# Kernel optimization log

Measured on AMD Instinct MI355X. Metric: run time of the kernel, lower is better.

Reference implementation:

```python
import jax, jax.numpy as jnp
import numpy as np

B, L, D_MODEL = 4, 4096, 1024
D_STATE = 16
DT_RANK = D_MODEL // 16  # 64
K = 4  # conv kernel size
EPS = 1e-5


def setup_inputs() -> dict:
    key = jax.random.key(0)
    ks = jax.random.split(key, 8)
    s = 0.02
    f = jax.random.normal(ks[0], (B, L, D_MODEL), dtype=jnp.float32)
    ln_g = jnp.ones((D_MODEL,), jnp.float32)
    ln_b = jnp.zeros((D_MODEL,), jnp.float32)
    Wx = jax.random.normal(ks[1], (D_MODEL, D_MODEL), jnp.float32) * s
    bx = jnp.zeros((D_MODEL,), jnp.float32)
    conv_w = jax.random.normal(ks[2], (D_MODEL, K), jnp.float32) * 0.1
    conv_b = jax.random.normal(ks[3], (D_MODEL,), jnp.float32) * s
    Wxp = jax.random.normal(ks[4], (D_MODEL, DT_RANK + 2 * D_STATE), jnp.float32) * s
    Wdt = jax.random.normal(ks[5], (DT_RANK, D_MODEL), jnp.float32) * s
    # negative bias keeps delta small so the (non-exponentiated) recurrence
    # h = (delta*A)*h + ... stays stable over L=4096 steps (|delta*A| < 1)
    bdt = jnp.full((D_MODEL,), -4.0, jnp.float32)
    A_log = jnp.tile(jnp.log(jnp.arange(1, D_STATE + 1, dtype=jnp.float32)), (D_MODEL, 1))
    Dp = jnp.ones((D_MODEL,), jnp.float32)
    return {"f": f, "ln_g": ln_g, "ln_b": ln_b, "Wx": Wx, "bx": bx,
            "conv_w": conv_w, "conv_b": conv_b, "Wxp": Wxp, "Wdt": Wdt,
            "bdt": bdt, "A_log": A_log, "Dp": Dp}


def reference(f, ln_g, ln_b, Wx, bx, conv_w, conv_b, Wxp, Wdt, bdt, A_log, Dp):
    b, l, d = f.shape
    # LayerNorm
    mu = jnp.mean(f, axis=-1, keepdims=True)
    var = jnp.mean(jnp.square(f - mu), axis=-1, keepdims=True)
    fn = (f - mu) * jax.lax.rsqrt(var + EPS) * ln_g + ln_b
    # input projection
    x = fn @ Wx + bx  # (b, l, d)
    # depthwise causal conv1d (torch pad=3 both sides then truncate to l == left-pad 3)
    xp = jnp.pad(x, ((0, 0), (K - 1, 0), (0, 0)))
    windows = jnp.stack([xp[:, k:k + l, :] for k in range(K)], axis=-1)  # (b, l, d, k)
    x = jnp.einsum('bldk,dk->bld', windows, conv_w) + conv_b
    x = jax.nn.silu(x)
    # selective SSM
    x_dbl = x @ Wxp  # (b, l, dt_rank + 2*n)
    dt = x_dbl[..., :DT_RANK]
    Bm = x_dbl[..., DT_RANK:DT_RANK + D_STATE]
    Cm = x_dbl[..., DT_RANK + D_STATE:]
    delta = jax.nn.softplus(dt @ Wdt + bdt)  # (b, l, d)
    A = -jnp.exp(A_log)  # (d, n)

    def step(h, inp):
        d_t, B_t, C_t, x_t = inp  # (b,d) (b,n) (b,n) (b,d)
        dA = d_t[:, :, None] * A                                  # (b, d, n)
        dB = (d_t * x_t)[:, :, None] * B_t[:, None, :]            # (b, d, n)
        h = dA * h + dB
        y = jnp.einsum('bdn,bn->bd', h, C_t)
        return h, y

    h0 = jnp.zeros((b, d, D_STATE), x.dtype)
    xs = (jnp.swapaxes(delta, 0, 1), jnp.swapaxes(Bm, 0, 1),
          jnp.swapaxes(Cm, 0, 1), jnp.swapaxes(x, 0, 1))
    _, ys = jax.lax.scan(step, h0, xs)  # ys: (l, b, d)
    y = jnp.swapaxes(ys, 0, 1) + x * Dp
    return y
```

## Files before the change

kernel.cpp:

```cpp
#include <hip/hip_runtime.h>
#include <cstdint>
#include <cstddef>

#define D_MODEL 1024
#define SEQ_L   4096
#define BATCH   4
#define NROWS   (BATCH*SEQ_L)
#define DSTATE  16
#define DTRANK  64
#define NDBL    96
#define CLEN    64
#define WARM    16
#define CT      16

typedef __attribute__((ext_vector_type(8))) _Float16 f16x8;
typedef __attribute__((ext_vector_type(4))) _Float16 h4;
typedef __attribute__((ext_vector_type(8))) _Float16 h8;
typedef __attribute__((ext_vector_type(4))) float f32x4;
typedef __attribute__((ext_vector_type(2))) float f32x2;

__device__ __forceinline__ float silu(float v) {
  return v / (1.f + __expf(-v));
}

__device__ __forceinline__ float softplus(float z) {
  return (z > 20.f) ? z : __logf(1.f + __expf(z));
}

__device__ __forceinline__ int swz64(int r, int e) { return e ^ ((r & 7) << 3); }

__global__ __launch_bounds__(256) void ln_kernel(const float* __restrict__ f,
                                                 const float* __restrict__ g,
                                                 const float* __restrict__ bta,
                                                 _Float16* __restrict__ fnb) {
  int row = blockIdx.x;
  int tid = threadIdx.x;
  const float* fr = f + (size_t)row * D_MODEL;
  float4 v = *(const float4*)&fr[tid * 4];
  float s  = v.x + v.y + v.z + v.w;
  float ss = v.x*v.x + v.y*v.y + v.z*v.z + v.w*v.w;
  #pragma unroll
  for (int o = 32; o > 0; o >>= 1) { s += __shfl_down(s, o); ss += __shfl_down(ss, o); }
  __shared__ float rs[8];
  int lane = tid & 63, w = tid >> 6;
  if (lane == 0) { rs[w] = s; rs[4 + w] = ss; }
  __syncthreads();
  if (tid == 0) {
    float S = rs[0] + rs[1] + rs[2] + rs[3];
    float SS = rs[4] + rs[5] + rs[6] + rs[7];
    float mu = S * (1.f / D_MODEL);
    float var = SS * (1.f / D_MODEL) - mu * mu;
    rs[0] = mu; rs[1] = rsqrtf(var + 1e-5f);
  }
  __syncthreads();
  float mu = rs[0], rstd = rs[1];
  float4 gv = *(const float4*)&g[tid * 4];
  float4 bv = *(const float4*)&bta[tid * 4];
  h4 o;
  o.x = (_Float16)((v.x - mu) * rstd * gv.x + bv.x);
  o.y = (_Float16)((v.y - mu) * rstd * gv.y + bv.y);
  o.z = (_Float16)((v.z - mu) * rstd * gv.z + bv.z);
  o.w = (_Float16)((v.w - mu) * rstd * gv.w + bv.w);
  *(h4*)&fnb[(size_t)row * D_MODEL + tid * 4] = o;
}

__global__ __launch_bounds__(256) void tcast(const float* __restrict__ W,
                                             _Float16* __restrict__ Wt,
                                             int rows, int cols) {
  __shared__ float tile[32][33];
  int tx = threadIdx.x & 31, ty = threadIdx.x >> 5;
  int c0 = blockIdx.x * 32, r0 = blockIdx.y * 32;
  #pragma unroll
  for (int i = 0; i < 4; ++i) {
    int r = ty + i * 8;
    tile[r][tx] = W[(size_t)(r0 + r) * cols + c0 + tx];
  }
  __syncthreads();
  #pragma unroll
  for (int i = 0; i < 4; ++i) {
    int n = ty + i * 8;
    Wt[(size_t)(c0 + n) * rows + r0 + tx] = (_Float16)tile[tx][n];
  }
}

__global__ __launch_bounds__(256, 4) void gemm1(const _Float16* __restrict__ Ab,
                                                const _Float16* __restrict__ Bt,
                                                const float* __restrict__ bias,
                                                _Float16* __restrict__ C) {
  __shared__ __align__(16) _Float16 As[128 * 64];
  __shared__ __align__(16) _Float16 Bs[128 * 64];
  const int K = D_MODEL, N = D_MODEL;
  int tid = threadIdx.x;
  int row0 = blockIdx.x * 128;
  int col0 = blockIdx.y * 128;
  int wave = tid >> 6, lane = tid & 63;
  int wr = wave >> 1, wc = wave & 1;
  int lr = lane & 15, half = lane >> 4;
  f32x4 acc[4][4] = {};

  int r_[4], gofs[4], wofs[4];
  #pragma unroll
  for (int i = 0; i < 4; ++i) {
    int c = tid + i * 256;
    int r = c >> 3, kc = c & 7;
    r_[i] = r;
    gofs[i] = kc * 8;
    wofs[i] = r * 64 + ((kc ^ (r & 7)) * 8);
  }

  for (int ks = 0; ks < 16; ++ks) {
    int k0 = ks * 64;
    h8 av[4], bv[4];
    #pragma unroll
    for (int i = 0; i < 4; ++i) {
      av[i] = *(const h8*)&Ab[(size_t)(row0 + r_[i]) * K + k0 + gofs[i]];
      bv[i] = *(const h8*)&Bt[(size_t)(col0 + r_[i]) * K + k0 + gofs[i]];
    }
    __syncthreads();
    #pragma unroll
    for (int i = 0; i < 4; ++i) {
      *(h8*)&As[wofs[i]] = av[i];
      *(h8*)&Bs[wofs[i]] = bv[i];
    }
    __syncthreads();
    #pragma unroll
    for (int kk = 0; kk < 2; ++kk) {
      int kch = ((kk * 4 + half) ^ (lr & 7)) * 8;
      f16x8 a[4], b[4];
      #pragma unroll
      for (int m = 0; m < 4; ++m)
        a[m] = *(const f16x8*)&As[(wr * 64 + m * 16 + lr) * 64 + kch];
      #pragma unroll
      for (int n = 0; n < 4; ++n)
        b[n] = *(const f16x8*)&Bs[(wc * 64 + n * 16 + lr) * 64 + kch];
      #pragma unroll
      for (int m = 0; m < 4; ++m)
        #pragma unroll
        for (int n = 0; n < 4; ++n)
          acc[m][n] = __builtin_amdgcn_mfma_f32_16x16x32_f16(b[n], a[m], acc[m][n], 0, 0, 0);
    }
  }
  #pragma unroll
  for (int m = 0; m < 4; ++m) {
    int gr = row0 + wr * 64 + m * 16 + lr;
    #pragma unroll
    for (int n = 0; n < 4; ++n) {
      int gc = col0 + wc * 64 + n * 16 + half * 4;
      float4 bv4 = *(const float4*)&bias[gc];
      h4 o;
      o.x = (_Float16)(acc[m][n][0] + bv4.x);
      o.y = (_Float16)(acc[m][n][1] + bv4.y);
      o.z = (_Float16)(acc[m][n][2] + bv4.z);
      o.w = (_Float16)(acc[m][n][3] + bv4.w);
      *(h4*)&C[(size_t)gr * N + gc] = o;
    }
  }
}

__global__ __launch_bounds__(256) void conv_silu(const _Float16* __restrict__ xlin,
                                                 const float* __restrict__ cw,
                                                 const float* __restrict__ cb,
                                                 _Float16* __restrict__ xo) {
  int idx = blockIdx.x * 256 + threadIdx.x;
  int d8 = idx & 127;
  int tg = idx >> 7;
  int row0 = tg * CT;
  int l0 = row0 & (SEQ_L - 1);
  int d = d8 * 8;
  float w[8][4];
  #pragma unroll
  for (int j = 0; j < 8; ++j) {
    float4 t = *(const float4*)&cw[(d + j) * 4];
    w[j][0] = t.x; w[j][1] = t.y; w[j][2] = t.z; w[j][3] = t.w;
  }
  float bias[8];
  #pragma unroll
  for (int j = 0; j < 8; j += 4) {
    float4 cbv = *(const float4*)&cb[d + j];
    bias[j] = cbv.x; bias[j+1] = cbv.y; bias[j+2] = cbv.z; bias[j+3] = cbv.w;
  }
  float win0[8], win1[8], win2[8];
  if (l0 == 0) {
    #pragma unroll
    for (int j = 0; j < 8; ++j) { win0[j] = 0.f; win1[j] = 0.f; win2[j] = 0.f; }
  } else {
    h8 m3 = *(const h8*)&xlin[(size_t)(row0 - 3) * D_MODEL + d];
    h8 m2 = *(const h8*)&xlin[(size_t)(row0 - 2) * D_MODEL + d];
    h8 m1 = *(const h8*)&xlin[(size_t)(row0 - 1) * D_MODEL + d];
    #pragma unroll
    for (int j = 0; j < 8; ++j) { win0[j] = (float)m3[j]; win1[j] = (float)m2[j]; win2[j] = (float)m1[j]; }
  }
  #pragma unroll
  for (int tt = 0; tt < CT; tt += 4) {
    h8 ld[4];
    #pragma unroll
    for (int k = 0; k < 4; ++k)
      ld[k] = *(const h8*)&xlin[(size_t)(row0 + tt + k) * D_MODEL + d];
    #pragma unroll
    for (int k = 0; k < 4; ++k) {
      float cur[8];
      #pragma unroll
      for (int j = 0; j < 8; ++j) cur[j] = (float)ld[k][j];
      h8 o;
      #pragma unroll
      for (int j = 0; j < 8; ++j) {
        float v = bias[j] + win0[j]*w[j][0] + win1[j]*w[j][1] + win2[j]*w[j][2] + cur[j]*w[j][3];
        o[j] = (_Float16)silu(v);
      }
      *(h8*)&xo[(size_t)(row0 + tt + k) * D_MODEL + d] = o;
      #pragma unroll
      for (int j = 0; j < 8; ++j) { win0[j] = win1[j]; win1[j] = win2[j]; win2[j] = cur[j]; }
    }
  }
}

__global__ __launch_bounds__(256) void gemm2(const _Float16* __restrict__ X,
                                             const _Float16* __restrict__ WT,
                                             float* __restrict__ Y) {
  __shared__ __align__(16) _Float16 As[64 * 64];
  __shared__ __align__(16) _Float16 Bs[96 * 64];
  int tid = threadIdx.x;
  int row0 = blockIdx.x * 64;
  int wave = tid >> 6, lane = tid & 63;
  int lr = lane & 15, half = lane >> 4;
  f32x4 acc[6] = {};
  for (int k0 = 0; k0 < D_MODEL; k0 += 64) {
    __syncthreads();
    #pragma unroll
    for (int i = 0; i < 2; ++i) {
      int cc = tid + i * 256;
      int r = cc >> 3, ko = (cc & 7) * 8;
      *(h8*)&As[r * 64 + swz64(r, ko)] = *(const h8*)&X[(size_t)(row0 + r) * D_MODEL + k0 + ko];
    }
    #pragma unroll
    for (int i = 0; i < 3; ++i) {
      int cc = tid + i * 256;
      int r = cc >> 3, ko = (cc & 7) * 8;
      *(h8*)&Bs[r * 64 + swz64(r, ko)] = *(const h8*)&WT[(size_t)r * D_MODEL + k0 + ko];
    }
    __syncthreads();
    #pragma unroll
    for (int kk = 0; kk < 2; ++kk) {
      f16x8 a = *(const f16x8*)&As[(wave * 16 + lr) * 64 + swz64(lr, kk * 32 + half * 8)];
      #pragma unroll
      for (int n = 0; n < 6; ++n) {
        f16x8 b = *(const f16x8*)&Bs[(n * 16 + lr) * 64 + swz64(lr, kk * 32 + half * 8)];
        acc[n] = __builtin_amdgcn_mfma_f32_16x16x32_f16(b, a, acc[n], 0, 0, 0);
      }
    }
  }
  int gr = row0 + wave * 16 + lr;
  #pragma unroll
  for (int n = 0; n < 6; ++n) {
    int gc = n * 16 + half * 4;
    *(f32x4*)&Y[(size_t)gr * NDBL + gc] = acc[n];
  }
}

__global__ __launch_bounds__(256) void gemm3(const float* __restrict__ XD,
                                             const _Float16* __restrict__ WT,
                                             const float* __restrict__ bdt,
                                             _Float16* __restrict__ Dl) {
  __shared__ __align__(16) _Float16 As[128 * 64];
  __shared__ __align__(16) _Float16 Bs[128 * 64];
  int tid = threadIdx.x;
  int row0 = blockIdx.x * 128;
  int col0 = blockIdx.y * 128;
  int wave = tid >> 6, lane = tid & 63;
  int wr = wave >> 1, wc = wave & 1;
  int lr = lane & 15, half = lane >> 4;
  #pragma unroll
  for (int i = 0; i < 8; ++i) {
    int cc = tid + i * 256;
    int r = cc >> 4, ko = (cc & 15) * 4;
    float4 v = *(const float4*)&XD[(size_t)(row0 + r) * NDBL + ko];
    h4 o; o.x = (_Float16)v.x; o.y = (_Float16)v.y; o.z = (_Float16)v.z; o.w = (_Float16)v.w;
    *(h4*)&As[r * 64 + swz64(r, ko)] = o;
  }
  #pragma unroll
  for (int i = 0; i < 4; ++i) {
    int cc = tid + i * 256;
    int r = cc >> 3, ko = (cc & 7) * 8;
    *(h8*)&Bs[r * 64 + swz64(r, ko)] = *(const h8*)&WT[(size_t)(col0 + r) * DTRANK + ko];
  }
  __syncthreads();
  f32x4 acc[4][4] = {};
  #pragma unroll
  for (int kk = 0; kk < 2; ++kk) {
    f16x8 a[4], b[4];
    #pragma unroll
    for (int m = 0; m < 4; ++m)
      a[m] = *(const f16x8*)&As[(wr * 64 + m * 16 + lr) * 64 + swz64(lr, kk * 32 + half * 8)];
    #pragma unroll
    for (int n = 0; n < 4; ++n)
      b[n] = *(const f16x8*)&Bs[(wc * 64 + n * 16 + lr) * 64 + swz64(lr, kk * 32 + half * 8)];
    #pragma unroll
    for (int m = 0; m < 4; ++m)
      #pragma unroll
      for (int n = 0; n < 4; ++n)
        acc[m][n] = __builtin_amdgcn_mfma_f32_16x16x32_f16(b[n], a[m], acc[m][n], 0, 0, 0);
  }
  #pragma unroll
  for (int m = 0; m < 4; ++m) {
    int gr = row0 + wr * 64 + m * 16 + lr;
    #pragma unroll
    for (int n = 0; n < 4; ++n) {
      int gc = col0 + wc * 64 + n * 16 + half * 4;
      float4 bv = *(const float4*)&bdt[gc];
      h4 o;
      o.x = (_Float16)softplus(acc[m][n][0] + bv.x);
      o.y = (_Float16)softplus(acc[m][n][1] + bv.y);
      o.z = (_Float16)softplus(acc[m][n][2] + bv.z);
      o.w = (_Float16)softplus(acc[m][n][3] + bv.w);
      *(h4*)&Dl[(size_t)gr * D_MODEL + gc] = o;
    }
  }
}

__global__ __launch_bounds__(256) void scan(const _Float16* __restrict__ delta,
                                            const _Float16* __restrict__ x,
                                            const float* __restrict__ xdbl,
                                            const float* __restrict__ A_log,
                                            const float* __restrict__ Dp,
                                            float* __restrict__ out) {
  int c = blockIdx.x, b = blockIdx.y, dq = blockIdx.z;
  int tid = threadIdx.x;
  int d = dq * 256 + tid;
  int warm = (c == 0) ? 0 : WARM;
  int t0 = c * CLEN - warm;
  int nt = CLEN + warm;
  __shared__ __align__(16) float Bl[(CLEN + WARM) * 16];
  __shared__ __align__(16) float Cl[(CLEN + WARM) * 16];
  int rowbase = b * SEQ_L + t0;
  for (int i = tid; i < nt * 4; i += 256) {
    int t = i >> 2, no = (i & 3) * 4;
    *(float4*)&Bl[t * 16 + no] = *(const float4*)&xdbl[(size_t)(rowbase + t) * NDBL + DTRANK + no];
    *(float4*)&Cl[t * 16 + no] = *(const float4*)&xdbl[(size_t)(rowbase + t) * NDBL + DTRANK + DSTATE + no];
  }
  __syncthreads();
  f32x2 Ar2[8], h2[8];
  #pragma unroll
  for (int q = 0; q < 4; ++q) {
    float4 al = *(const float4*)&A_log[d * 16 + q * 4];
    Ar2[q*2+0] = (f32x2){-__expf(al.x), -__expf(al.y)};
    Ar2[q*2+1] = (f32x2){-__expf(al.z), -__expf(al.w)};
  }
  #pragma unroll
  for (int q = 0; q < 8; ++q) h2[q] = (f32x2){0.f, 0.f};
  float dpv = Dp[d];
  const _Float16* dp_ = delta + (size_t)rowbase * D_MODEL + d;
  const _Float16* xp_ = x + (size_t)rowbase * D_MODEL + d;
  float* op_ = out + (size_t)rowbase * D_MODEL + d;

  float dA[16], xA[16], dB[16], xB[16];
  auto issue = [&](float (&db)[16], float (&xb)[16], int tbase) {
    #pragma unroll
    for (int k = 0; k < 16; ++k) {
      db[k] = (float)dp_[(size_t)(tbase + k) * D_MODEL];
      xb[k] = (float)xp_[(size_t)(tbase + k) * D_MODEL];
    }
  };
  auto compute = [&](float (&db)[16], float (&xb)[16], int tbase) {
    #pragma unroll
    for (int k = 0; k < 16; ++k) {
      int t = tbase + k;
      float dlt = db[k], xv = xb[k];
      float dx = dlt * xv;
      f32x2 dlt2 = (f32x2){dlt, dlt};
      f32x2 dx2  = (f32x2){dx, dx};
      f32x2 y2   = (f32x2){0.f, 0.f};
      const float4* Bp = (const float4*)&Bl[t * 16];
      const float4* Cp = (const float4*)&Cl[t * 16];
      #pragma unroll
      for (int q = 0; q < 4; ++q) {
        float4 bq = Bp[q];
        float4 cq = Cp[q];
        f32x2 blo = (f32x2){bq.x, bq.y}, bhi = (f32x2){bq.z, bq.w};
        f32x2 clo = (f32x2){cq.x, cq.y}, chi = (f32x2){cq.z, cq.w};
        f32x2 a0 = dlt2 * Ar2[q*2+0];
        f32x2 a1 = dlt2 * Ar2[q*2+1];
        h2[q*2+0] = a0 * h2[q*2+0] + dx2 * blo;
        h2[q*2+1] = a1 * h2[q*2+1] + dx2 * bhi;
        y2 = y2 + h2[q*2+0] * clo;
        y2 = y2 + h2[q*2+1] * chi;
      }
      if (t >= warm)
        __builtin_nontemporal_store(y2[0] + y2[1] + xv * dpv, &op_[(size_t)t * D_MODEL]);
    }
  };

  issue(dA, xA, 0);
  int tb = 0;
  while (true) {
    if (tb + 16 < nt) issue(dB, xB, tb + 16);
    compute(dA, xA, tb);
    tb += 16;
    if (tb >= nt) break;
    if (tb + 16 < nt) issue(dA, xA, tb + 16);
    compute(dB, xB, tb);
    tb += 16;
    if (tb >= nt) break;
  }
}

extern "C" void kernel_launch(void* const* d_in, const int* in_sizes, int n_in,
                              void* d_out, int out_size, void* d_ws, size_t ws_size,
                              hipStream_t stream) {
  const float* f     = (const float*)d_in[0];
  const float* ln_g  = (const float*)d_in[1];
  const float* ln_b  = (const float*)d_in[2];
  const float* Wx    = (const float*)d_in[3];
  const float* bx    = (const float*)d_in[4];
  const float* convw = (const float*)d_in[5];
  const float* convb = (const float*)d_in[6];
  const float* Wxp   = (const float*)d_in[7];
  const float* Wdt   = (const float*)d_in[8];
  const float* bdt   = (const float*)d_in[9];
  const float* A_log = (const float*)d_in[10];
  const float* Dp    = (const float*)d_in[11];
  float* out = (float*)d_out;
  char* ws = (char*)d_ws;

  _Float16* fnb  = (_Float16*)(ws);
  _Float16* xlin = (_Float16*)(ws + 33554432);
  _Float16* xbuf = (_Float16*)(ws + 67108864);
  float*    xdbl = (float*)(ws + 100663296);
  _Float16* wxt  = (_Float16*)(ws + 106954752);
  _Float16* wxpT = (_Float16*)(ws + 109051904);
  _Float16* wdtT = (_Float16*)(ws + 109248512);
  _Float16* delta = xlin;

  tcast<<<dim3(32, 32), dim3(256), 0, stream>>>(Wx, wxt, 1024, 1024);
  tcast<<<dim3(3, 32),  dim3(256), 0, stream>>>(Wxp, wxpT, 1024, 96);
  tcast<<<dim3(32, 2),  dim3(256), 0, stream>>>(Wdt, wdtT, 64, 1024);
  ln_kernel<<<dim3(NROWS), dim3(256), 0, stream>>>(f, ln_g, ln_b, fnb);
  gemm1<<<dim3(NROWS / 128, D_MODEL / 128), dim3(256), 0, stream>>>(fnb, wxt, bx, xlin);
  conv_silu<<<dim3((NROWS / CT) * (D_MODEL / 8) / 256), dim3(256), 0, stream>>>(xlin, convw, convb, xbuf);
  gemm2<<<dim3(NROWS / 64), dim3(256), 0, stream>>>(xbuf, wxpT, xdbl);
  gemm3<<<dim3(NROWS / 128, D_MODEL / 128), dim3(256), 0, stream>>>(xdbl, wdtT, bdt, delta);
  scan<<<dim3(SEQ_L / CLEN, BATCH, 4), dim3(256), 0, stream>>>(delta, xbuf, xdbl, A_log, Dp, out);
}
```

Before: 164.3 us.

## Stage GEMM tiles and scan delta/x inputs via direct global-to-LDS loads

The gemm1 tile loads now use global_load_lds 16-byte transfers straight into shared memory instead of going through registers. The XOR swizzle moves to the global read address so that each lane's LDS destination stays contiguous. The scan kernel drops its per-thread strided 2-byte register prefetch of delta and x. It now stages 16-timestep blocks of both into double-buffered LDS with coalesced 16-byte direct loads, which should cut global transaction count and register pressure. The cost is an extra barrier per block, plus reliance on the barrier fence waiting for the async LDS DMA to complete.

```diff
diff --git a/kernel.cpp b/kernel.cpp
--- a/kernel.cpp
+++ b/kernel.cpp
@@ -12,12 +12,20 @@
 #define CLEN    64
 #define WARM    16
 #define CT      16
+#define SBLK    16
 
 typedef __attribute__((ext_vector_type(8))) _Float16 f16x8;
 typedef __attribute__((ext_vector_type(4))) _Float16 h4;
 typedef __attribute__((ext_vector_type(8))) _Float16 h8;
 typedef __attribute__((ext_vector_type(4))) float f32x4;
 typedef __attribute__((ext_vector_type(2))) float f32x2;
+
+typedef __attribute__((address_space(1))) const unsigned int* as1_u32p;
+typedef __attribute__((address_space(3))) unsigned int* as3_u32p;
+
+__device__ __forceinline__ void gload16(const void* g, void* l) {
+  __builtin_amdgcn_global_load_lds((as1_u32p)g, (as3_u32p)l, 16, 0, 0);
+}
 
 __device__ __forceinline__ float silu(float v) {
   return v / (1.f + __expf(-v));
@@ -98,29 +106,23 @@
   int lr = lane & 15, half = lane >> 4;
   f32x4 acc[4][4] = {};
 
-  int r_[4], gofs[4], wofs[4];
+  int r_[4], sofs[4], ldso[4];
   #pragma unroll
   for (int i = 0; i < 4; ++i) {
     int c = tid + i * 256;
     int r = c >> 3, kc = c & 7;
     r_[i] = r;
-    gofs[i] = kc * 8;
-    wofs[i] = r * 64 + ((kc ^ (r & 7)) * 8);
+    sofs[i] = ((kc ^ (r & 7)) * 8);
+    ldso[i] = c * 8;
   }
 
   for (int ks = 0; ks < 16; ++ks) {
     int k0 = ks * 64;
-    h8 av[4], bv[4];
+    __syncthreads();
     #pragma unroll
     for (int i = 0; i < 4; ++i) {
-      av[i] = *(const h8*)&Ab[(size_t)(row0 + r_[i]) * K + k0 + gofs[i]];
-      bv[i] = *(const h8*)&Bt[(size_t)(col0 + r_[i]) * K + k0 + gofs[i]];
-    }
-    __syncthreads();
-    #pragma unroll
-    for (int i = 0; i < 4; ++i) {
-      *(h8*)&As[wofs[i]] = av[i];
-      *(h8*)&Bs[wofs[i]] = bv[i];
+      gload16(&Ab[(size_t)(row0 + r_[i]) * K + k0 + sofs[i]], &As[ldso[i]]);
+      gload16(&Bt[(size_t)(col0 + r_[i]) * K + k0 + sofs[i]], &Bs[ldso[i]]);
     }
     __syncthreads();
     #pragma unroll
@@ -331,13 +333,14 @@
   int nt = CLEN + warm;
   __shared__ __align__(16) float Bl[(CLEN + WARM) * 16];
   __shared__ __align__(16) float Cl[(CLEN + WARM) * 16];
+  __shared__ __align__(16) _Float16 dl[2][SBLK * 256];
+  __shared__ __align__(16) _Float16 xl[2][SBLK * 256];
   int rowbase = b * SEQ_L + t0;
   for (int i = tid; i < nt * 4; i += 256) {
     int t = i >> 2, no = (i & 3) * 4;
     *(float4*)&Bl[t * 16 + no] = *(const float4*)&xdbl[(size_t)(rowbase + t) * NDBL + DTRANK + no];
     *(float4*)&Cl[t * 16 + no] = *(const float4*)&xdbl[(size_t)(rowbase + t) * NDBL + DTRANK + DSTATE + no];
   }
-  __syncthreads();
   f32x2 Ar2[8], h2[8];
   #pragma unroll
   for (int q = 0; q < 4; ++q) {
@@ -348,23 +351,31 @@
   #pragma unroll
   for (int q = 0; q < 8; ++q) h2[q] = (f32x2){0.f, 0.f};
   float dpv = Dp[d];
-  const _Float16* dp_ = delta + (size_t)rowbase * D_MODEL + d;
-  const _Float16* xp_ = x + (size_t)rowbase * D_MODEL + d;
+  const _Float16* dp0 = delta + (size_t)rowbase * D_MODEL + dq * 256;
+  const _Float16* xp0 = x     + (size_t)rowbase * D_MODEL + dq * 256;
   float* op_ = out + (size_t)rowbase * D_MODEL + d;
 
-  float dA[16], xA[16], dB[16], xB[16];
-  auto issue = [&](float (&db)[16], float (&xb)[16], int tbase) {
-    #pragma unroll
-    for (int k = 0; k < 16; ++k) {
-      db[k] = (float)dp_[(size_t)(tbase + k) * D_MODEL];
-      xb[k] = (float)xp_[(size_t)(tbase + k) * D_MODEL];
-    }
-  };
-  auto compute = [&](float (&db)[16], float (&xb)[16], int tbase) {
-    #pragma unroll
-    for (int k = 0; k < 16; ++k) {
-      int t = tbase + k;
-      float dlt = db[k], xv = xb[k];
+#define STAGE(buf, ts)                                                         \
+  {                                                                            \
+    _Pragma("unroll")                                                          \
+    for (int i_ = 0; i_ < 2; ++i_) {                                           \
+      int c2 = tid + i_ * 256;                                                 \
+      int tr_ = c2 >> 5, tc_ = (c2 & 31) * 8;                                  \
+      gload16(&dp0[(size_t)((ts) + tr_) * D_MODEL + tc_], &dl[buf][c2 * 8]);   \
+      gload16(&xp0[(size_t)((ts) + tr_) * D_MODEL + tc_], &xl[buf][c2 * 8]);   \
+    }                                                                          \
+  }
+
+  STAGE(0, 0)
+  int cur = 0;
+  for (int tb = 0; tb < nt; tb += SBLK) {
+    __syncthreads();
+    if (tb + SBLK < nt) STAGE(cur ^ 1, tb + SBLK)
+    #pragma unroll
+    for (int k = 0; k < SBLK; ++k) {
+      int t = tb + k;
+      float dlt = (float)dl[cur][k * 256 + tid];
+      float xv  = (float)xl[cur][k * 256 + tid];
       float dx = dlt * xv;
       f32x2 dlt2 = (f32x2){dlt, dlt};
       f32x2 dx2  = (f32x2){dx, dx};
@@ -387,20 +398,9 @@
       if (t >= warm)
         __builtin_nontemporal_store(y2[0] + y2[1] + xv * dpv, &op_[(size_t)t * D_MODEL]);
     }
-  };
-
-  issue(dA, xA, 0);
-  int tb = 0;
-  while (true) {
-    if (tb + 16 < nt) issue(dB, xB, tb + 16);
-    compute(dA, xA, tb);
-    tb += 16;
-    if (tb >= nt) break;
-    if (tb + 16 < nt) issue(dA, xA, tb + 16);
-    compute(dB, xB, tb);
-    tb += 16;
-    if (tb >= nt) break;
-  }
+    cur ^= 1;
+  }
+#undef STAGE
 }
 
 extern "C" void kernel_launch(void* const* d_in, const int* in_sizes, int n_in,
```

After: 162.5 us. Within noise of the previous version (-1.1%).
